# Kernel tuning notes

Measured on AMD Instinct MI355X. Metric: run time of the kernel, lower is better.

## Reference

```python
import jax, jax.numpy as jnp
import numpy as np

DIM = 10
V_CH = 5
P = 50176  # 224*224
C = 4
B = 64
TEMPERATURE = 10.0
LN_EPS = 1e-5


def _mlp_ln(x, w1, b1, w2, b2, g, beta):
    # Linear(dim,128) + LeakyReLU(0.1) + Linear(128,16) + LayerNorm(16)
    h = x @ w1.T + b1
    h = jnp.where(h >= 0, h, 0.1 * h)
    h = h @ w2.T + b2
    mu = jnp.mean(h, axis=-1, keepdims=True)
    var = jnp.mean((h - mu) ** 2, axis=-1, keepdims=True)
    return (h - mu) / jnp.sqrt(var + LN_EPS) * g + beta


def setup_inputs() -> dict:
    key = jax.random.key(0)
    ks = jax.random.split(key, 10)
    inp = {
        'q': jax.random.normal(ks[0], (B, DIM, 1), jnp.float32),
        'k': jax.random.normal(ks[1], (B, DIM, 1, C), jnp.float32),
        'v': jax.random.normal(ks[2], (B, V_CH, P, C), jnp.float32),
        'modality_dropout': jax.random.randint(ks[3], (B, C), 0, 2).astype(jnp.float32),
        'q_w1': jax.random.normal(ks[4], (128, DIM), jnp.float32) * 0.1,
        'q_b1': jnp.zeros((128,), jnp.float32),
        'q_w2': jax.random.normal(ks[5], (16, 128), jnp.float32) * 0.1,
        'q_b2': jnp.zeros((16,), jnp.float32),
        'q_g': jnp.ones((16,), jnp.float32),
        'q_beta': jnp.zeros((16,), jnp.float32),
        'k_w1': jax.random.normal(ks[6], (128, DIM), jnp.float32) * 0.1,
        'k_b1': jnp.zeros((128,), jnp.float32),
        'k_w2': jax.random.normal(ks[7], (16, 128), jnp.float32) * 0.1,
        'k_b2': jnp.zeros((16,), jnp.float32),
        'k_g': jnp.ones((16,), jnp.float32),
        'k_beta': jnp.zeros((16,), jnp.float32),
    }
    return inp


def reference(q, k, v, modality_dropout,
              q_w1, q_b1, q_w2, q_b2, q_g, q_beta,
              k_w1, k_b1, k_w2, k_b2, k_g, k_beta):
    b, _, num_q = q.shape
    num_v = v.shape[2]
    image_dim = int(np.sqrt(num_v))  # 224
    qe = _mlp_ln(q[:, :, 0], q_w1, q_b1, q_w2, q_b2, q_g, q_beta)            # (B,16)
    ke = _mlp_ln(jnp.transpose(k[:, :, 0, :], (0, 2, 1)),
                 k_w1, k_b1, k_w2, k_b2, k_g, k_beta)                         # (B,C,16)
    scale = DIM ** (-0.5)
    logits = jnp.einsum('bd,bcd->bc', qe, ke) * scale                         # (B,C)
    # num_q_patches == 1, so the logit is constant over space; dropout mask then softmax
    logits = logits - modality_dropout * 1e5
    attn = jax.nn.softmax(logits / TEMPERATURE, axis=-1)                      # (B,C)
    out = jnp.einsum('bc,bvpc->bvp', attn, v).reshape(b, V_CH, image_dim, image_dim)
    attn_map = jnp.broadcast_to(attn[:, :, None, None], (b, C, image_dim, image_dim))
    return out, attn_map
```

## Files before the change

kernel.cpp:

```cpp
#include <hip/hip_runtime.h>
#include <math.h>

#define B 64
#define DIM 10
#define V_CH 5
#define P 50176
#define C 4

typedef float f32x4 __attribute__((ext_vector_type(4)));

__global__ __launch_bounds__(128) void attn_kernel(
    const float* __restrict__ q,
    const float* __restrict__ k,
    const float* __restrict__ md,
    const float* __restrict__ qw1, const float* __restrict__ qb1,
    const float* __restrict__ qw2, const float* __restrict__ qb2,
    const float* __restrict__ qg,  const float* __restrict__ qbeta,
    const float* __restrict__ kw1, const float* __restrict__ kb1,
    const float* __restrict__ kw2, const float* __restrict__ kb2,
    const float* __restrict__ kg,  const float* __restrict__ kbeta,
    float* __restrict__ attn)
{
    const int b = blockIdx.x;
    const int t = threadIdx.x;

    __shared__ float xs[DIM];
    __shared__ float h1s[128];
    __shared__ float h2s[16];
    __shared__ float e[5][16];
    __shared__ float lg[4];

    for (int h = 0; h < 5; ++h) {
        const float *w1, *b1, *w2, *b2, *g, *beta;
        if (h == 0) { w1 = qw1; b1 = qb1; w2 = qw2; b2 = qb2; g = qg; beta = qbeta; }
        else        { w1 = kw1; b1 = kb1; w2 = kw2; b2 = kb2; g = kg; beta = kbeta; }

        if (t < DIM) {
            xs[t] = (h == 0) ? q[b * DIM + t]
                             : k[(b * DIM + t) * C + (h - 1)];
        }
        __syncthreads();

        {
            float acc = b1[t];
            #pragma unroll
            for (int d = 0; d < DIM; ++d) acc += w1[t * DIM + d] * xs[d];
            h1s[t] = (acc >= 0.f) ? acc : 0.1f * acc;
        }
        __syncthreads();

        if (t < 16) {
            float acc = b2[t];
            #pragma unroll
            for (int i = 0; i < 128; ++i) acc += w2[t * 128 + i] * h1s[i];
            h2s[t] = acc;
        }
        __syncthreads();

        if (t < 16) {
            float mu = 0.f;
            #pragma unroll
            for (int j = 0; j < 16; ++j) mu += h2s[j];
            mu *= (1.f / 16.f);
            float var = 0.f;
            #pragma unroll
            for (int j = 0; j < 16; ++j) { float d = h2s[j] - mu; var += d * d; }
            var *= (1.f / 16.f);
            e[h][t] = (h2s[t] - mu) / sqrtf(var + 1e-5f) * g[t] + beta[t];
        }
        __syncthreads();
    }

    if (t < C) {
        float d = 0.f;
        #pragma unroll
        for (int j = 0; j < 16; ++j) d += e[0][j] * e[1 + t][j];
        lg[t] = d * 0.31622776601683794f - md[b * C + t] * 1e5f;
    }
    __syncthreads();

    if (t < C) {
        float m = fmaxf(fmaxf(lg[0], lg[1]), fmaxf(lg[2], lg[3])) * 0.1f;
        float s = 0.f;
        #pragma unroll
        for (int c = 0; c < C; ++c) s += expf(lg[c] * 0.1f - m);
        attn[b * C + t] = expf(lg[t] * 0.1f - m) / s;
    }
}

__global__ __launch_bounds__(256) void wsum_kernel(
    const f32x4* __restrict__ v4,
    const float* __restrict__ attn,
    float* __restrict__ out)
{
    const int y = blockIdx.y;
    const int t = threadIdx.x;

    if (y < B * V_CH) {
        const int b = y / V_CH;
        const f32x4 a = *(const f32x4*)(attn + b * C);
        const size_t base = (size_t)y * P + (size_t)blockIdx.x * 1024;
        #pragma unroll
        for (int i = 0; i < 4; ++i) {
            const int p = i * 256 + t;
            const f32x4 vv = __builtin_nontemporal_load(v4 + base + p);
            const float r = vv.x * a.x + vv.y * a.y + vv.z * a.z + vv.w * a.w;
            __builtin_nontemporal_store(r, out + base + p);
        }
    } else {
        const int idx = y - B * V_CH;
        const float val = attn[idx];
        const size_t off = (size_t)(B * V_CH) * P + (size_t)idx * P
                         + (size_t)blockIdx.x * 1024 + (size_t)t * 4;
        const f32x4 r = { val, val, val, val };
        __builtin_nontemporal_store(r, (f32x4*)(out + off));
    }
}

extern "C" void kernel_launch(void* const* d_in, const int* in_sizes, int n_in,
                              void* d_out, int out_size, void* d_ws, size_t ws_size,
                              hipStream_t stream) {
    const float* q     = (const float*)d_in[0];
    const float* k     = (const float*)d_in[1];
    const float* v     = (const float*)d_in[2];
    const float* md    = (const float*)d_in[3];
    const float* qw1   = (const float*)d_in[4];
    const float* qb1   = (const float*)d_in[5];
    const float* qw2   = (const float*)d_in[6];
    const float* qb2   = (const float*)d_in[7];
    const float* qg    = (const float*)d_in[8];
    const float* qbeta = (const float*)d_in[9];
    const float* kw1   = (const float*)d_in[10];
    const float* kb1   = (const float*)d_in[11];
    const float* kw2   = (const float*)d_in[12];
    const float* kb2   = (const float*)d_in[13];
    const float* kg    = (const float*)d_in[14];
    const float* kbeta = (const float*)d_in[15];

    float* attn = (float*)d_ws;
    float* out  = (float*)d_out;

    attn_kernel<<<B, 128, 0, stream>>>(q, k, md,
                                       qw1, qb1, qw2, qb2, qg, qbeta,
                                       kw1, kb1, kw2, kb2, kg, kbeta,
                                       attn);

    dim3 grid(49, B * V_CH + B * C);
    wsum_kernel<<<grid, 256, 0, stream>>>((const f32x4*)v, attn, out);
}
```

Baseline: 405.2 us.

## Fuse attention MLP into weighted-sum kernel with per-block recompute and prefetch

Merges the two kernels into one launch. Every block recomputes the small query/key MLP, LayerNorm and softmax for its batch instead of reading attention weights that a separate kernel wrote first. Each block issues its first v load before that computation so the load overlaps it. Work is regrouped into 7 larger chunks per (batch, channel) row, with a loop over 28 vectors per thread. This removes a launch and the dependency between kernels, but adds redundant MLP work and several barriers to every block.

Measured after the change: 420.0 us. +3.7%, slower.

```diff
diff --git a/kernel.cpp b/kernel.cpp
--- a/kernel.cpp
+++ b/kernel.cpp
@@ -7,11 +7,17 @@
 #define P 50176
 #define C 4
 
+#define XCH 7
+#define CHUNK (P / XCH)
+#define NWSUM (B * V_CH * XCH)
+#define NMAP  (B * C * XCH)
+
 typedef float f32x4 __attribute__((ext_vector_type(4)));
 
-__global__ __launch_bounds__(128) void attn_kernel(
+__global__ __launch_bounds__(256) void fused_kernel(
     const float* __restrict__ q,
     const float* __restrict__ k,
+    const f32x4* __restrict__ v4,
     const float* __restrict__ md,
     const float* __restrict__ qw1, const float* __restrict__ qb1,
     const float* __restrict__ qw2, const float* __restrict__ qb2,
@@ -19,16 +25,31 @@
     const float* __restrict__ kw1, const float* __restrict__ kb1,
     const float* __restrict__ kw2, const float* __restrict__ kb2,
     const float* __restrict__ kg,  const float* __restrict__ kbeta,
-    float* __restrict__ attn)
+    float* __restrict__ out)
 {
-    const int b = blockIdx.x;
-    const int t = threadIdx.x;
+    const int blk = blockIdx.x;
+    const int t   = threadIdx.x;
+
+    const bool is_map = (blk >= NWSUM);
+    int idx, ch, b;
+    if (!is_map) {
+        idx = blk / XCH; ch = blk % XCH; b = idx / V_CH;
+    } else {
+        const int m = blk - NWSUM;
+        idx = m / XCH; ch = m % XCH; b = idx / C;
+    }
+
+    const size_t wbase = (size_t)idx * P + (size_t)ch * CHUNK;
+
+    f32x4 pre = {0.f, 0.f, 0.f, 0.f};
+    if (!is_map) pre = __builtin_nontemporal_load(v4 + wbase + t);
 
     __shared__ float xs[DIM];
     __shared__ float h1s[128];
     __shared__ float h2s[16];
     __shared__ float e[5][16];
     __shared__ float lg[4];
+    __shared__ float as[4];
 
     for (int h = 0; h < 5; ++h) {
         const float *w1, *b1, *w2, *b2, *g, *beta;
@@ -41,7 +62,7 @@
         }
         __syncthreads();
 
-        {
+        if (t < 128) {
             float acc = b1[t];
             #pragma unroll
             for (int d = 0; d < DIM; ++d) acc += w1[t * DIM + d] * xs[d];
@@ -84,36 +105,29 @@
         float s = 0.f;
         #pragma unroll
         for (int c = 0; c < C; ++c) s += expf(lg[c] * 0.1f - m);
-        attn[b * C + t] = expf(lg[t] * 0.1f - m) / s;
+        as[t] = expf(lg[t] * 0.1f - m) / s;
     }
-}
+    __syncthreads();
 
-__global__ __launch_bounds__(256) void wsum_kernel(
-    const f32x4* __restrict__ v4,
-    const float* __restrict__ attn,
-    float* __restrict__ out)
-{
-    const int y = blockIdx.y;
-    const int t = threadIdx.x;
-
-    if (y < B * V_CH) {
-        const int b = y / V_CH;
-        const f32x4 a = *(const f32x4*)(attn + b * C);
-        const size_t base = (size_t)y * P + (size_t)blockIdx.x * 1024;
-        #pragma unroll
-        for (int i = 0; i < 4; ++i) {
+    if (!is_map) {
+        const f32x4 a = { as[0], as[1], as[2], as[3] };
+        {
+            const float r = pre.x * a.x + pre.y * a.y + pre.z * a.z + pre.w * a.w;
+            __builtin_nontemporal_store(r, out + wbase + t);
+        }
+        for (int i = 1; i < CHUNK / 256; ++i) {
             const int p = i * 256 + t;
-            const f32x4 vv = __builtin_nontemporal_load(v4 + base + p);
+            const f32x4 vv = __builtin_nontemporal_load(v4 + wbase + p);
             const float r = vv.x * a.x + vv.y * a.y + vv.z * a.z + vv.w * a.w;
-            __builtin_nontemporal_store(r, out + base + p);
+            __builtin_nontemporal_store(r, out + wbase + p);
         }
     } else {
-        const int idx = y - B * V_CH;
-        const float val = attn[idx];
-        const size_t off = (size_t)(B * V_CH) * P + (size_t)idx * P
-                         + (size_t)blockIdx.x * 1024 + (size_t)t * 4;
+        const float val = as[idx & 3];
+        float* mp = out + (size_t)(B * V_CH) * P + wbase;
         const f32x4 r = { val, val, val, val };
-        __builtin_nontemporal_store(r, (f32x4*)(out + off));
+        #pragma unroll
+        for (int i = 0; i < CHUNK / 1024; ++i)
+            __builtin_nontemporal_store(r, (f32x4*)mp + i * 256 + t);
     }
 }
 
@@ -137,14 +151,9 @@
     const float* kg    = (const float*)d_in[14];
     const float* kbeta = (const float*)d_in[15];
 
-    float* attn = (float*)d_ws;
-    float* out  = (float*)d_out;
-
-    attn_kernel<<<B, 128, 0, stream>>>(q, k, md,
-                                       qw1, qb1, qw2, qb2, qg, qbeta,
-                                       kw1, kb1, kw2, kb2, kg, kbeta,
-                                       attn);
-
-    dim3 grid(49, B * V_CH + B * C);
-    wsum_kernel<<<grid, 256, 0, stream>>>((const f32x4*)v, attn, out);
+    fused_kernel<<<NWSUM + NMAP, 256, 0, stream>>>(
+        q, k, (const f32x4*)v, md,
+        qw1, qb1, qw2, qb2, qg, qbeta,
+        kw1, kb1, kw2, kb2, kg, kbeta,
+        (float*)d_out);
 }
```
